# Kernel optimization log

Hardware: AMD Instinct MI355X
Metric: run time of the kernel (lower is better)

Reference implementation:

```python
import jax, jax.numpy as jnp
import numpy as np

NEG_SLOPE = 0.01
NUM_GRAPHS = 4096


def _gcn(x, W, b, src, dst, ew, n_nodes):
    # GCNConv(normalize=False): linear transform, then weighted scatter-add to targets, plus bias
    h = x @ W                                  # [N, out]
    msg = h[src] * ew[:, None]                 # [E, out] gather + scale
    agg = jax.ops.segment_sum(msg, dst, num_segments=n_nodes)  # scatter-add
    return agg + b


def setup_inputs() -> dict:
    key = jax.random.key(0)
    ks = jax.random.split(key, 24)
    N, E = 253952, 4000000
    x = jax.random.normal(ks[0], (N, 6), dtype=jnp.float32)
    edge_index = jax.random.randint(ks[1], (2, E), 0, N, dtype=jnp.int64)
    edge_weight = jax.random.uniform(ks[2], (E,), dtype=jnp.float32)
    batch = jnp.sort(jax.random.randint(ks[3], (N,), 0, NUM_GRAPHS, dtype=jnp.int64))

    def lin(k, fi, fo):
        k1, k2 = jax.random.split(k)
        s = 1.0 / np.sqrt(fi)
        return (jax.random.normal(k1, (fi, fo), dtype=jnp.float32) * s,
                jax.random.normal(k2, (fo,), dtype=jnp.float32) * s)

    W1, b1 = lin(ks[4], 6, 16)
    W2, b2 = lin(ks[5], 16, 32)
    W3, b3 = lin(ks[6], 32, 64)
    W4, b4 = lin(ks[7], 64, 50)
    Wf1, bf1 = lin(ks[8], 50, 30)
    Wf2, bf2 = lin(ks[9], 30, 20)
    Wf3, bf3 = lin(ks[10], 20, 2)
    return {"x": x, "edge_index": edge_index, "edge_weight": edge_weight, "batch": batch,
            "W1": W1, "b1": b1, "W2": W2, "b2": b2, "W3": W3, "b3": b3, "W4": W4, "b4": b4,
            "Wf1": Wf1, "bf1": bf1, "Wf2": Wf2, "bf2": bf2, "Wf3": Wf3, "bf3": bf3}


def reference(x, edge_index, edge_weight, batch,
              W1, b1, W2, b2, W3, b3, W4, b4,
              Wf1, bf1, Wf2, bf2, Wf3, bf3):
    lrelu = lambda v: jax.nn.leaky_relu(v, NEG_SLOPE)
    src, dst = edge_index[0], edge_index[1]
    n = x.shape[0]
    h = lrelu(_gcn(x, W1, b1, src, dst, edge_weight, n))
    h = lrelu(_gcn(h, W2, b2, src, dst, edge_weight, n))
    h = lrelu(_gcn(h, W3, b3, src, dst, edge_weight, n))
    conv_out = lrelu(_gcn(h, W4, b4, src, dst, edge_weight, n))
    # original applies leaky_relu again (batch_norm is defined but never used)
    h = lrelu(conv_out)
    pooled = jax.ops.segment_sum(h, batch, num_segments=NUM_GRAPHS)  # global_add_pool -> [G, 50]
    out = lrelu(pooled @ Wf1 + bf1)
    # dropout p=0.2 skipped (eval mode)
    out = lrelu(out @ Wf2 + bf2)
    out = lrelu(out @ Wf3 + bf3)
    return out
```

## Files before the change

### kernel.cpp

```cpp
#include <hip/hip_runtime.h>

#define N_NODES 253952
#define N_EDGES 4000000
#define N_GRAPHS 4096
#define NEG_SLOPE 0.01f

#define NB   248
#define CAP  20480
#define EPB  4096
#define WSCALE (1.0f / 16383.0f)

__device__ __forceinline__ float lrelu(float v) {
    return v > 0.0f ? v : v * NEG_SLOPE;
}

__device__ __forceinline__ unsigned short f2bf(float f) {
    unsigned b = __float_as_uint(f);
    return (unsigned short)((b + 0x7FFF + ((b >> 16) & 1)) >> 16);
}

__device__ __forceinline__ float bf2f(unsigned short h) {
    return __uint_as_float((unsigned)h << 16);
}

__device__ __forceinline__ void fma_bf16x8(float acc[8], const uint4 v, const float w) {
    acc[0] += __uint_as_float(v.x << 16) * w;
    acc[1] += __uint_as_float(v.x & 0xFFFF0000u) * w;
    acc[2] += __uint_as_float(v.y << 16) * w;
    acc[3] += __uint_as_float(v.y & 0xFFFF0000u) * w;
    acc[4] += __uint_as_float(v.z << 16) * w;
    acc[5] += __uint_as_float(v.z & 0xFFFF0000u) * w;
    acc[6] += __uint_as_float(v.w << 16) * w;
    acc[7] += __uint_as_float(v.w & 0xFFFF0000u) * w;
}

__global__ void pad_x_kernel(const float* __restrict__ x, unsigned short* __restrict__ xb,
                             int* __restrict__ bucket_cnt) {
    if (blockIdx.x == 0 && threadIdx.x < NB) bucket_cnt[threadIdx.x] = 0;
    int i = blockIdx.x * 256 + threadIdx.x;
    if (i >= N_NODES * 8) return;
    int n = i >> 3, j = i & 7;
    xb[i] = (j < 6) ? f2bf(x[n * 6 + j]) : (unsigned short)0;
}

__global__ void partA_kernel(const int* __restrict__ src, const int* __restrict__ dst,
                             const float* __restrict__ ew,
                             int* __restrict__ bucket_cnt, int2* __restrict__ staging) {
    __shared__ int cnt[NB], base[NB], cur[NB];
    for (int i = threadIdx.x; i < NB; i += 256) cnt[i] = 0;
    __syncthreads();
    const int e0 = blockIdx.x * EPB;
    int s[16], d[16]; float w[16];
#pragma unroll
    for (int k = 0; k < 16; ++k) {
        int e = e0 + k * 256 + threadIdx.x;
        if (e < N_EDGES) { s[k] = src[e]; d[k] = dst[e]; w[k] = ew[e]; }
        else d[k] = -1;
    }
#pragma unroll
    for (int k = 0; k < 16; ++k)
        if (d[k] >= 0) atomicAdd(&cnt[d[k] >> 10], 1);
    __syncthreads();
    for (int i = threadIdx.x; i < NB; i += 256) {
        int c = cnt[i];
        base[i] = (c > 0) ? atomicAdd(&bucket_cnt[i], c) : 0;
        cur[i] = 0;
    }
    __syncthreads();
#pragma unroll
    for (int k = 0; k < 16; ++k) {
        if (d[k] >= 0) {
            int b = d[k] >> 10;
            int off = atomicAdd(&cur[b], 1);
            staging[(size_t)b * CAP + base[b] + off] =
                make_int2(s[k] | ((d[k] & 1023) << 18), __float_as_int(w[k]));
        }
    }
}

__global__ void __launch_bounds__(1024)
partB_kernel(const int2* __restrict__ staging,
             const int* __restrict__ bucket_cnt,
             int* __restrict__ row_start, unsigned* __restrict__ csr) {
    __shared__ int hist[1024];
    __shared__ int s[1024];
    __shared__ int s_bbase;
    const int b = blockIdx.x;
    const int t = threadIdx.x;
    int v = (t < 256) ? ((t < NB) ? bucket_cnt[t] : 0) : 0;
    if (t < 256) s[t] = v;
    __syncthreads();
    for (int off = 1; off < 256; off <<= 1) {
        int tv = (t < 256 && t >= off) ? s[t - off] : 0;
        __syncthreads();
        if (t < 256) s[t] += tv;
        __syncthreads();
    }
    if (t == b) s_bbase = s[t] - v;
    if (b == 0 && t == 0) row_start[N_NODES] = N_EDGES;
    hist[t] = 0;
    __syncthreads();
    const int bbase = s_bbase;
    const int cnt = bucket_cnt[b];
    const int2* rec = staging + (size_t)b * CAP;
    for (int i = t; i < cnt; i += 1024)
        atomicAdd(&hist[rec[i].x >> 18], 1);
    __syncthreads();
    int h = hist[t];
    s[t] = h;
    __syncthreads();
    for (int off = 1; off < 1024; off <<= 1) {
        int tv = (t >= off) ? s[t - off] : 0;
        __syncthreads();
        s[t] += tv;
        __syncthreads();
    }
    int excl = s[t] - h;
    row_start[b * 1024 + t] = bbase + excl;
    hist[t] = excl;
    __syncthreads();
    for (int i = t; i < cnt; i += 1024) {
        int2 r = rec[i];
        int dl = r.x >> 18;
        int pos = bbase + atomicAdd(&hist[dl], 1);
        int wq = (int)(__int_as_float(r.y) * 16383.0f + 0.5f);
        wq = wq < 0 ? 0 : (wq > 16383 ? 16383 : wq);
        csr[pos] = (unsigned)(r.x & 0x3FFFF) | ((unsigned)wq << 18);
    }
}

template <int WPAD, int WIN, int WOUT, bool DBL, bool OUT_F32>
__global__ void gcn_layer_kernel(const unsigned short* __restrict__ xb,
                                 const unsigned* __restrict__ csr,
                                 const int* __restrict__ row_start, const int* __restrict__ row_end,
                                 const float* __restrict__ Wg, const float* __restrict__ bg,
                                 void* __restrict__ hout) {
    constexpr int LPN = WPAD / 8;
    constexpr int GROUPS = 256 / LPN;
    __shared__ float rows[GROUPS][WPAD + 4];
    int g = threadIdx.x / LPN;
    int j = threadIdx.x % LPN;
    int node = blockIdx.x * GROUPS + g;
    float acc[8] = {0.f, 0.f, 0.f, 0.f, 0.f, 0.f, 0.f, 0.f};
    int e = row_start[node];
    int end = row_end[node];
    const uint4* xv = (const uint4*)xb;
    for (; e + 4 <= end; e += 4) {
        unsigned r0 = csr[e];
        unsigned r1 = csr[e + 1];
        unsigned r2 = csr[e + 2];
        unsigned r3 = csr[e + 3];
        uint4 v0 = xv[(size_t)(r0 & 0x3FFFFu) * LPN + j];
        uint4 v1 = xv[(size_t)(r1 & 0x3FFFFu) * LPN + j];
        uint4 v2 = xv[(size_t)(r2 & 0x3FFFFu) * LPN + j];
        uint4 v3 = xv[(size_t)(r3 & 0x3FFFFu) * LPN + j];
        fma_bf16x8(acc, v0, (float)(r0 >> 18) * WSCALE);
        fma_bf16x8(acc, v1, (float)(r1 >> 18) * WSCALE);
        fma_bf16x8(acc, v2, (float)(r2 >> 18) * WSCALE);
        fma_bf16x8(acc, v3, (float)(r3 >> 18) * WSCALE);
    }
    for (; e < end; ++e) {
        unsigned r = csr[e];
        uint4 v = xv[(size_t)(r & 0x3FFFFu) * LPN + j];
        fma_bf16x8(acc, v, (float)(r >> 18) * WSCALE);
    }
#pragma unroll
    for (int i = 0; i < 8; ++i) rows[g][8 * j + i] = acc[i];
    __syncthreads();
    for (int idx = threadIdx.x; idx < GROUPS * WOUT; idx += 256) {
        int g2 = idx / WOUT;
        int j2 = idx - g2 * WOUT;
        int node2 = blockIdx.x * GROUPS + g2;
        float a = bg[j2];
#pragma unroll
        for (int k = 0; k < WIN; ++k) a += rows[g2][k] * Wg[k * WOUT + j2];
        a = lrelu(a);
        if (DBL) a = lrelu(a);
        if (OUT_F32) ((float*)hout)[(size_t)node2 * WOUT + j2] = a;
        else ((unsigned short*)hout)[(size_t)node2 * WOUT + j2] = f2bf(a);
    }
}

__global__ void pool_kernel(const unsigned short* __restrict__ h,
                            const int* __restrict__ batch,
                            float* __restrict__ pooled) {
    int g = blockIdx.x;
    __shared__ int s_start, s_end;
    if (threadIdx.x == 0) {
        int lo = 0, hi = N_NODES;
        while (lo < hi) { int m = (lo + hi) >> 1; if (batch[m] < g) lo = m + 1; else hi = m; }
        s_start = lo;
        lo = 0; hi = N_NODES;
        while (lo < hi) { int m = (lo + hi) >> 1; if (batch[m] < g + 1) lo = m + 1; else hi = m; }
        s_end = lo;
    }
    __syncthreads();
    int j = threadIdx.x;
    if (j < 50) {
        float acc = 0.0f;
        for (int i = s_start; i < s_end; ++i) acc += bf2f(h[(size_t)i * 50 + j]);
        pooled[g * 50 + j] = acc;
    }
}

__global__ void mlp_kernel(const float* __restrict__ pooled,
                           const float* __restrict__ Wf1, const float* __restrict__ bf1,
                           const float* __restrict__ Wf2, const float* __restrict__ bf2,
                           const float* __restrict__ Wf3, const float* __restrict__ bf3,
                           float* __restrict__ out) {
    __shared__ float W1s[50 * 30], b1s[30];
    __shared__ float W2s[30 * 20], b2s[20];
    __shared__ float W3s[20 * 2], b3s[2];
    for (int i = threadIdx.x; i < 50 * 30; i += blockDim.x) W1s[i] = Wf1[i];
    for (int i = threadIdx.x; i < 30; i += blockDim.x) b1s[i] = bf1[i];
    for (int i = threadIdx.x; i < 30 * 20; i += blockDim.x) W2s[i] = Wf2[i];
    for (int i = threadIdx.x; i < 20; i += blockDim.x) b2s[i] = bf2[i];
    for (int i = threadIdx.x; i < 20 * 2; i += blockDim.x) W3s[i] = Wf3[i];
    for (int i = threadIdx.x; i < 2; i += blockDim.x) b3s[i] = bf3[i];
    __syncthreads();
    int g = blockIdx.x * blockDim.x + threadIdx.x;
    if (g >= N_GRAPHS) return;
    float in[50];
#pragma unroll
    for (int k = 0; k < 50; ++k) in[k] = pooled[g * 50 + k];
    float t1[30];
#pragma unroll
    for (int j = 0; j < 30; ++j) {
        float a = b1s[j];
#pragma unroll
        for (int k = 0; k < 50; ++k) a += in[k] * W1s[k * 30 + j];
        t1[j] = lrelu(a);
    }
    float t2[20];
#pragma unroll
    for (int j = 0; j < 20; ++j) {
        float a = b2s[j];
#pragma unroll
        for (int k = 0; k < 30; ++k) a += t1[k] * W2s[k * 20 + j];
        t2[j] = lrelu(a);
    }
#pragma unroll
    for (int j = 0; j < 2; ++j) {
        float a = b3s[j];
#pragma unroll
        for (int k = 0; k < 20; ++k) a += t2[k] * W3s[k * 2 + j];
        out[g * 2 + j] = lrelu(a);
    }
}

extern "C" void kernel_launch(void* const* d_in, const int* in_sizes, int n_in,
                              void* d_out, int out_size, void* d_ws, size_t ws_size,
                              hipStream_t stream) {
    const float* x     = (const float*)d_in[0];
    const int*   ei    = (const int*)d_in[1];
    const float* ew    = (const float*)d_in[2];
    const int*   batch = (const int*)d_in[3];
    const float* W1 = (const float*)d_in[4];
    const float* b1 = (const float*)d_in[5];
    const float* W2 = (const float*)d_in[6];
    const float* b2 = (const float*)d_in[7];
    const float* W3 = (const float*)d_in[8];
    const float* b3 = (const float*)d_in[9];
    const float* W4 = (const float*)d_in[10];
    const float* b4 = (const float*)d_in[11];
    const float* Wf1 = (const float*)d_in[12];
    const float* bf1 = (const float*)d_in[13];
    const float* Wf2 = (const float*)d_in[14];
    const float* bf2 = (const float*)d_in[15];
    const float* Wf3 = (const float*)d_in[16];
    const float* bf3 = (const float*)d_in[17];

    const int* src = ei;
    const int* dst = ei + N_EDGES;
    float* out = (float*)d_out;

    char* wsp = (char*)d_ws;
    unsigned* csr     = (unsigned*)wsp;  wsp += (size_t)N_EDGES * 4;
    char*  bufA       = wsp;             wsp += (size_t)N_NODES * 64 * 4;
    char*  bufB       = wsp;             wsp += (size_t)N_NODES * 50 * 4;
    int*   row_start  = (int*)wsp;       wsp += (size_t)(N_NODES + 1) * 4;
    int*   bucket_cnt = (int*)wsp;       wsp += NB * 4;
    float* pooled     = (float*)wsp;

    int2*           staging = (int2*)bufA;
    unsigned short* xb      = (unsigned short*)bufB;
    unsigned short* h1      = (unsigned short*)bufA;
    unsigned short* h2      = (unsigned short*)(bufB + (size_t)N_NODES * 8 * 2);
    unsigned short* h3      = (unsigned short*)bufA;
    unsigned short* h4      = (unsigned short*)bufB;

    const int BS = 256;
    const int ABLK = (N_EDGES + EPB - 1) / EPB;

    pad_x_kernel<<<(N_NODES * 8 + 255) / 256, BS, 0, stream>>>(x, xb, bucket_cnt);
    partA_kernel<<<ABLK, BS, 0, stream>>>(src, dst, ew, bucket_cnt, staging);
    partB_kernel<<<NB, 1024, 0, stream>>>(staging, bucket_cnt, row_start, csr);

    gcn_layer_kernel<8, 6, 16, false, false><<<N_NODES / 256, BS, 0, stream>>>(
        xb, csr, row_start, row_start + 1, W1, b1, h1);
    gcn_layer_kernel<16, 16, 32, false, false><<<N_NODES / 128, BS, 0, stream>>>(
        h1, csr, row_start, row_start + 1, W2, b2, h2);
    gcn_layer_kernel<32, 32, 64, false, false><<<N_NODES / 64, BS, 0, stream>>>(
        h2, csr, row_start, row_start + 1, W3, b3, h3);
    gcn_layer_kernel<64, 64, 50, true, false><<<N_NODES / 32, BS, 0, stream>>>(
        h3, csr, row_start, row_start + 1, W4, b4, h4);

    pool_kernel<<<N_GRAPHS, 64, 0, stream>>>(h4, batch, pooled);
    mlp_kernel<<<(N_GRAPHS + 255) / 256, 256, 0, stream>>>(pooled, Wf1, bf1, Wf2, bf2, Wf3, bf3, out);
}
```

Baseline: 699.9 us.

## Locally sort edges in LDS before staging writes; vectorize loads and use wave-shuffle scan

The bucketing kernel now loads src/dst/weight with 128-bit vector loads. Each block counting-sorts its 4096 edges by bucket in shared memory, then writes them out contiguously per bucket, so staging writes coalesce instead of scattering. The CSR build kernel reads staging records in pairs as int4 and replaces the 1024-wide shared-memory Hillis-Steele scan with a wave-level shuffle scan. The cost is extra shared memory (32KB sort buffer), a per-element binary search to find each record's bucket, and more barriers in the bucketing kernel.

New measurement: 685.7 us. 2.0% less time.

```diff
diff --git a/kernel.cpp b/kernel.cpp
--- a/kernel.cpp
+++ b/kernel.cpp
@@ -46,35 +46,77 @@
 __global__ void partA_kernel(const int* __restrict__ src, const int* __restrict__ dst,
                              const float* __restrict__ ew,
                              int* __restrict__ bucket_cnt, int2* __restrict__ staging) {
-    __shared__ int cnt[NB], base[NB], cur[NB];
-    for (int i = threadIdx.x; i < NB; i += 256) cnt[i] = 0;
+    __shared__ int cnt[NB];
+    __shared__ int lds_base[NB + 1];
+    __shared__ int gbase[NB];
+    __shared__ int cur[NB];
+    __shared__ int ss[256];
+    __shared__ int2 sorted[EPB];
+    const int t = threadIdx.x;
+    for (int i = t; i < NB; i += 256) cnt[i] = 0;
     __syncthreads();
     const int e0 = blockIdx.x * EPB;
-    int s[16], d[16]; float w[16];
-#pragma unroll
-    for (int k = 0; k < 16; ++k) {
-        int e = e0 + k * 256 + threadIdx.x;
-        if (e < N_EDGES) { s[k] = src[e]; d[k] = dst[e]; w[k] = ew[e]; }
-        else d[k] = -1;
-    }
-#pragma unroll
-    for (int k = 0; k < 16; ++k)
-        if (d[k] >= 0) atomicAdd(&cnt[d[k] >> 10], 1);
-    __syncthreads();
-    for (int i = threadIdx.x; i < NB; i += 256) {
-        int c = cnt[i];
-        base[i] = (c > 0) ? atomicAdd(&bucket_cnt[i], c) : 0;
-        cur[i] = 0;
-    }
-    __syncthreads();
-#pragma unroll
-    for (int k = 0; k < 16; ++k) {
-        if (d[k] >= 0) {
-            int b = d[k] >> 10;
-            int off = atomicAdd(&cur[b], 1);
-            staging[(size_t)b * CAP + base[b] + off] =
-                make_int2(s[k] | ((d[k] & 1023) << 18), __float_as_int(w[k]));
+    int4 s4[4]; int4 d4[4]; float4 w4[4];
+#pragma unroll
+    for (int k = 0; k < 4; ++k) {
+        int e = e0 + 4 * (k * 256 + t);
+        if (e + 3 < N_EDGES) {
+            s4[k] = *(const int4*)(src + e);
+            d4[k] = *(const int4*)(dst + e);
+            w4[k] = *(const float4*)(ew + e);
+        } else {
+            s4[k] = make_int4(0, 0, 0, 0);
+            d4[k] = make_int4(-1, -1, -1, -1);
+            w4[k] = make_float4(0.f, 0.f, 0.f, 0.f);
+            if (e < N_EDGES)     { s4[k].x = src[e];     d4[k].x = dst[e];     w4[k].x = ew[e]; }
+            if (e + 1 < N_EDGES) { s4[k].y = src[e + 1]; d4[k].y = dst[e + 1]; w4[k].y = ew[e + 1]; }
+            if (e + 2 < N_EDGES) { s4[k].z = src[e + 2]; d4[k].z = dst[e + 2]; w4[k].z = ew[e + 2]; }
         }
+    }
+#pragma unroll
+    for (int k = 0; k < 4; ++k) {
+        if (d4[k].x >= 0) atomicAdd(&cnt[d4[k].x >> 10], 1);
+        if (d4[k].y >= 0) atomicAdd(&cnt[d4[k].y >> 10], 1);
+        if (d4[k].z >= 0) atomicAdd(&cnt[d4[k].z >> 10], 1);
+        if (d4[k].w >= 0) atomicAdd(&cnt[d4[k].w >> 10], 1);
+    }
+    __syncthreads();
+    int v = (t < NB) ? cnt[t] : 0;
+    ss[t] = v;
+    __syncthreads();
+    for (int off = 1; off < 256; off <<= 1) {
+        int tv = (t >= off) ? ss[t - off] : 0;
+        __syncthreads();
+        ss[t] += tv;
+        __syncthreads();
+    }
+    if (t < NB) {
+        int excl = ss[t] - v;
+        lds_base[t] = excl;
+        cur[t] = excl;
+        gbase[t] = (v > 0) ? atomicAdd(&bucket_cnt[t], v) : 0;
+    }
+    if (t == 255) lds_base[NB] = ss[255];
+    __syncthreads();
+#pragma unroll
+    for (int k = 0; k < 4; ++k) {
+        int d, s; float w;
+        d = d4[k].x; s = s4[k].x; w = w4[k].x;
+        if (d >= 0) sorted[atomicAdd(&cur[d >> 10], 1)] = make_int2(s | ((d & 1023) << 18), __float_as_int(w));
+        d = d4[k].y; s = s4[k].y; w = w4[k].y;
+        if (d >= 0) sorted[atomicAdd(&cur[d >> 10], 1)] = make_int2(s | ((d & 1023) << 18), __float_as_int(w));
+        d = d4[k].z; s = s4[k].z; w = w4[k].z;
+        if (d >= 0) sorted[atomicAdd(&cur[d >> 10], 1)] = make_int2(s | ((d & 1023) << 18), __float_as_int(w));
+        d = d4[k].w; s = s4[k].w; w = w4[k].w;
+        if (d >= 0) sorted[atomicAdd(&cur[d >> 10], 1)] = make_int2(s | ((d & 1023) << 18), __float_as_int(w));
+    }
+    __syncthreads();
+    const int total = lds_base[NB];
+    for (int p = t; p < total; p += 256) {
+        int2 r = sorted[p];
+        int lo = 0, hi = NB - 1;
+        while (lo < hi) { int m = (lo + hi + 1) >> 1; if (lds_base[m] <= p) lo = m; else hi = m - 1; }
+        staging[(size_t)lo * CAP + gbase[lo] + (p - lds_base[lo])] = r;
     }
 }
 
@@ -83,46 +125,74 @@
              const int* __restrict__ bucket_cnt,
              int* __restrict__ row_start, unsigned* __restrict__ csr) {
     __shared__ int hist[1024];
-    __shared__ int s[1024];
+    __shared__ int ss[256];
+    __shared__ int wsum[16];
     __shared__ int s_bbase;
     const int b = blockIdx.x;
     const int t = threadIdx.x;
-    int v = (t < 256) ? ((t < NB) ? bucket_cnt[t] : 0) : 0;
-    if (t < 256) s[t] = v;
+    int v = 0;
+    if (t < 256) { v = (t < NB) ? bucket_cnt[t] : 0; ss[t] = v; }
     __syncthreads();
     for (int off = 1; off < 256; off <<= 1) {
-        int tv = (t < 256 && t >= off) ? s[t - off] : 0;
+        int tv = (t < 256 && t >= off) ? ss[t - off] : 0;
         __syncthreads();
-        if (t < 256) s[t] += tv;
+        if (t < 256) ss[t] += tv;
         __syncthreads();
     }
-    if (t == b) s_bbase = s[t] - v;
+    if (t == b) s_bbase = ss[t] - v;
     if (b == 0 && t == 0) row_start[N_NODES] = N_EDGES;
     hist[t] = 0;
     __syncthreads();
     const int bbase = s_bbase;
     const int cnt = bucket_cnt[b];
     const int2* rec = staging + (size_t)b * CAP;
-    for (int i = t; i < cnt; i += 1024)
-        atomicAdd(&hist[rec[i].x >> 18], 1);
-    __syncthreads();
+    const int4* rec2 = (const int4*)rec;
+    const int npair = cnt >> 1;
+    for (int i = t; i < npair; i += 1024) {
+        int4 pr = rec2[i];
+        atomicAdd(&hist[pr.x >> 18], 1);
+        atomicAdd(&hist[pr.z >> 18], 1);
+    }
+    if ((cnt & 1) && t == 0) atomicAdd(&hist[rec[cnt - 1].x >> 18], 1);
+    __syncthreads();
+    const int lane = t & 63, wid = t >> 6;
     int h = hist[t];
-    s[t] = h;
-    __syncthreads();
-    for (int off = 1; off < 1024; off <<= 1) {
-        int tv = (t >= off) ? s[t - off] : 0;
-        __syncthreads();
-        s[t] += tv;
-        __syncthreads();
-    }
-    int excl = s[t] - h;
+    int val = h;
+#pragma unroll
+    for (int off = 1; off < 64; off <<= 1) {
+        int n = __shfl_up(val, off);
+        if (lane >= off) val += n;
+    }
+    if (lane == 63) wsum[wid] = val;
+    __syncthreads();
+    if (t < 16) {
+        int wv = wsum[t];
+#pragma unroll
+        for (int off = 1; off < 16; off <<= 1) {
+            int n = __shfl_up(wv, off);
+            if (t >= off) wv += n;
+        }
+        wsum[t] = wv;
+    }
+    __syncthreads();
+    int excl = val - h + (wid > 0 ? wsum[wid - 1] : 0);
     row_start[b * 1024 + t] = bbase + excl;
     hist[t] = excl;
     __syncthreads();
-    for (int i = t; i < cnt; i += 1024) {
-        int2 r = rec[i];
-        int dl = r.x >> 18;
-        int pos = bbase + atomicAdd(&hist[dl], 1);
+    for (int i = t; i < npair; i += 1024) {
+        int4 pr = rec2[i];
+        int p0 = bbase + atomicAdd(&hist[pr.x >> 18], 1);
+        int wq0 = (int)(__int_as_float(pr.y) * 16383.0f + 0.5f);
+        wq0 = wq0 < 0 ? 0 : (wq0 > 16383 ? 16383 : wq0);
+        csr[p0] = (unsigned)(pr.x & 0x3FFFF) | ((unsigned)wq0 << 18);
+        int p1 = bbase + atomicAdd(&hist[pr.z >> 18], 1);
+        int wq1 = (int)(__int_as_float(pr.w) * 16383.0f + 0.5f);
+        wq1 = wq1 < 0 ? 0 : (wq1 > 16383 ? 16383 : wq1);
+        csr[p1] = (unsigned)(pr.z & 0x3FFFF) | ((unsigned)wq1 << 18);
+    }
+    if ((cnt & 1) && t == 0) {
+        int2 r = rec[cnt - 1];
+        int pos = bbase + atomicAdd(&hist[r.x >> 18], 1);
         int wq = (int)(__int_as_float(r.y) * 16383.0f + 0.5f);
         wq = wq < 0 ? 0 : (wq > 16383 ? 16383 : wq);
         csr[pos] = (unsigned)(r.x & 0x3FFFF) | ((unsigned)wq << 18);
```
